# Kernel tuning notes

Hardware: AMD Instinct MI355X
Metric: run time of the kernel (lower is better)

Reference implementation:

```python
import jax, jax.numpy as jnp
import numpy as np

B, N, DIM, H, DH = 4, 2048, 1024, 16, 64

def setup_inputs() -> dict:
    key = jax.random.key(0)
    k1, k2, k3 = jax.random.split(key, 3)
    x = jax.random.normal(k1, (B, N, DIM), dtype=jnp.float32)
    mask = jnp.ones((B, N), dtype=bool)
    w_qkv = jax.random.normal(k2, (DIM, 3 * H * DH), dtype=jnp.float32) * (DIM ** -0.5)
    w_out = jax.random.normal(k3, (H * DH, DIM), dtype=jnp.float32) * ((H * DH) ** -0.5)
    b_out = jnp.zeros((DIM,), dtype=jnp.float32)
    return {"x": x, "mask": mask, "w_qkv": w_qkv, "w_out": w_out, "b_out": b_out}

def reference(x, mask, w_qkv, w_out, b_out):
    b, n, _ = x.shape
    h, dh = H, DH
    scale = dh ** -0.5
    qkv = x @ w_qkv  # [b, n, 3*h*dh]
    q, k, v = jnp.split(qkv, 3, axis=-1)
    # [b, n, h*dh] -> [b, h, n, dh]
    reshape = lambda t: t.reshape(b, n, h, dh).transpose(0, 2, 1, 3)
    q, k, v = reshape(q) * scale, reshape(k), reshape(v)
    dots = jnp.einsum('bhid,bhjd->bhij', q, k)  # materialized N x N scores
    neg = -jnp.finfo(dots.dtype).max
    # key padding mask: [b, j] -> [b, 1, 1, j]
    dots = jnp.where(mask[:, None, None, :], dots, neg)
    # causal mask: mask out j > i
    causal = jnp.triu(jnp.ones((n, n), dtype=bool), k=1)
    dots = jnp.where(causal[None, None, :, :], neg, dots)
    attn = jax.nn.softmax(dots, axis=-1)
    out = jnp.einsum('bhij,bhjd->bhid', attn, v)
    out = out.transpose(0, 2, 1, 3).reshape(b, n, h * dh)
    return out @ w_out + b_out
```

## Files before the change

kernel.cpp:

```cpp
#include <hip/hip_runtime.h>

#define B_   4
#define N_   2048
#define DIM_ 1024
#define H_   16
#define DH_  64
#define NT   (B_ * N_)
#define PS   ((size_t)B_ * H_ * N_ * DH_)

typedef __bf16 bf16x8 __attribute__((ext_vector_type(8)));
typedef short  s16x4  __attribute__((ext_vector_type(4)));
typedef float  f32x4  __attribute__((ext_vector_type(4)));
typedef unsigned int   u32;
typedef unsigned int   u32x2 __attribute__((ext_vector_type(2)));
typedef unsigned short u16;

#define LOG2E 1.44269504088896f
#define QSCALE (0.125f * LOG2E)

__device__ __forceinline__ u16 f2bf(float f) {
  u32 u = __float_as_uint(f);
  u += 0x7FFFu + ((u >> 16) & 1u);
  return (u16)(u >> 16);
}

__device__ __forceinline__ u32 bfpack(float f0, float f1) {
  u32 a = __float_as_uint(f0) + 0x8000u;
  u32 b = __float_as_uint(f1) + 0x8000u;
  return __builtin_amdgcn_perm(b, a, 0x07060302);
}

__device__ __forceinline__ float fexp2(float x) {
  return __builtin_amdgcn_exp2f(x);
}

__device__ __forceinline__ f32x4 mfma32(bf16x8 a, bf16x8 b, f32x4 c) {
  return __builtin_amdgcn_mfma_f32_16x16x32_bf16(a, b, c, 0, 0, 0);
}
__device__ __forceinline__ f32x4 mfma16k(s16x4 a, s16x4 b, f32x4 c) {
  return __builtin_amdgcn_mfma_f32_16x16x16bf16_1k(a, b, c, 0, 0, 0);
}

__device__ __forceinline__ void gld16(const void* g, void* l) {
  __builtin_amdgcn_global_load_lds(
      (const __attribute__((address_space(1))) u32*)g,
      (__attribute__((address_space(3))) u32*)l, 16, 0, 0);
}

__device__ __forceinline__ void transpose_body(
    const float* __restrict__ w, u16* __restrict__ wt,
    int K, int Ncols, int bx, int by, int tid, u16* T ) {
  const int n0 = bx * 64, k0 = by * 64;
  const int r = tid >> 4, c4 = (tid & 15) * 4;
#pragma unroll
  for (int i = 0; i < 4; ++i) {
    int row = r + i * 16;
    float4 f = *(const float4*)(w + (size_t)(k0 + row) * Ncols + n0 + c4);
    u16* p = &T[row * 66 + c4];
    p[0] = f2bf(f.x); p[1] = f2bf(f.y); p[2] = f2bf(f.z); p[3] = f2bf(f.w);
  }
  __syncthreads();
  const int nr = tid >> 2, kc = (tid & 3) * 16;
  u32 p[8];
#pragma unroll
  for (int j = 0; j < 8; ++j)
    p[j] = (u32)T[(kc + 2 * j) * 66 + nr] | ((u32)T[(kc + 2 * j + 1) * 66 + nr] << 16);
  size_t dst = (size_t)(n0 + nr) * K + k0 + kc;
  *(uint4*)(wt + dst)     = make_uint4(p[0], p[1], p[2], p[3]);
  *(uint4*)(wt + dst + 8) = make_uint4(p[4], p[5], p[6], p[7]);
}

__global__ __launch_bounds__(256) void prologue_kernel(
    const float* __restrict__ x, u16* __restrict__ xb,
    const float* __restrict__ w_qkv, u16* __restrict__ wqkvT,
    const float* __restrict__ w_out, u16* __restrict__ woutT) {
  __shared__ u16 T[64 * 66];
  const int b = blockIdx.x, tid = threadIdx.x;
  if (b < 4096) {
    size_t i = ((size_t)b * 256 + tid) * 8;
    float4 f0 = *(const float4*)(x + i);
    float4 f1 = *(const float4*)(x + i + 4);
    uint4 o;
    o.x = (u32)f2bf(f0.x) | ((u32)f2bf(f0.y) << 16);
    o.y = (u32)f2bf(f0.z) | ((u32)f2bf(f0.w) << 16);
    o.z = (u32)f2bf(f1.x) | ((u32)f2bf(f1.y) << 16);
    o.w = (u32)f2bf(f1.z) | ((u32)f2bf(f1.w) << 16);
    *(uint4*)(xb + i) = o;
  } else if (b < 4864) {
    int idx = b - 4096;
    transpose_body(w_qkv, wqkvT, 1024, 3072, idx % 48, idx / 48, tid, T);
  } else {
    int idx = b - 4864;
    transpose_body(w_out, woutT, 1024, 1024, idx % 16, idx / 16, tid, T);
  }
}

__global__ __launch_bounds__(256) void qkv_gemm_kernel(
    const u16* __restrict__ xb, const u16* __restrict__ wt,
    u16* __restrict__ q, u16* __restrict__ k, u16* __restrict__ vt) {
  __shared__ alignas(16) u16 As[2 * 128 * 64];
  __shared__ alignas(16) u16 Bs[2 * 128 * 64];
  const int tid = threadIdx.x, wave = tid >> 6, lane = tid & 63;
  const int quad = lane >> 4, l15 = lane & 15;
  const int wm = (wave >> 1) * 64, wn = (wave & 1) * 64;
  const int m0 = blockIdx.y * 128, n0 = blockIdx.x * 128;
  const int srow = lane >> 3;
  const int schunk = (lane & 7) ^ srow;

  const u16* asrc = xb + (size_t)(m0 + srow) * DIM_ + schunk * 8;
  const u16* bsrc = wt + (size_t)(n0 + srow) * DIM_ + schunk * 8;

  f32x4 acc[4][4] = {};

#pragma unroll
  for (int i = 0; i < 4; ++i) {
    int c = wave * 4 + i;
    gld16(asrc + (size_t)(c * 8) * DIM_, As + c * 512);
    gld16(bsrc + (size_t)(c * 8) * DIM_, Bs + c * 512);
  }

  for (int t = 0; t < 16; ++t) {
    if (t < 15) {
      int pn = (t + 1) & 1;
#pragma unroll
      for (int i = 0; i < 4; ++i) {
        int c = wave * 4 + i;
        gld16(asrc + (size_t)(c * 8) * DIM_ + (t + 1) * 64, As + pn * 8192 + c * 512);
        gld16(bsrc + (size_t)(c * 8) * DIM_ + (t + 1) * 64, Bs + pn * 8192 + c * 512);
      }
      asm volatile("s_waitcnt vmcnt(8)" ::: "memory");
    } else {
      asm volatile("s_waitcnt vmcnt(0)" ::: "memory");
    }
    __builtin_amdgcn_s_barrier();
    __builtin_amdgcn_sched_barrier(0);

    const u16* Ab = As + (t & 1) * 8192;
    const u16* Bb = Bs + (t & 1) * 8192;
#pragma unroll
    for (int h = 0; h < 2; ++h) {
      bf16x8 af[4], bfr[4];
#pragma unroll
      for (int mi = 0; mi < 4; ++mi) {
        int row = wm + mi * 16 + l15;
        af[mi] = *(const bf16x8*)(Ab + row * 64 + (((quad + 4 * h) ^ (row & 7)) * 8));
      }
#pragma unroll
      for (int ni = 0; ni < 4; ++ni) {
        int row = wn + ni * 16 + l15;
        bfr[ni] = *(const bf16x8*)(Bb + row * 64 + (((quad + 4 * h) ^ (row & 7)) * 8));
      }
#pragma unroll
      for (int ni = 0; ni < 4; ++ni)
#pragma unroll
        for (int mi = 0; mi < 4; ++mi)
          acc[mi][ni] = mfma32(af[mi], bfr[ni], acc[mi][ni]);
    }
    __builtin_amdgcn_sched_barrier(0);
    __builtin_amdgcn_s_barrier();
  }

#pragma unroll
  for (int ni = 0; ni < 4; ++ni) {
    int colg = n0 + wn + ni * 16 + l15;
    int part = colg >> 10, rem = colg & 1023;
    int hh = rem >> 6, d = rem & 63;
#pragma unroll
    for (int mi = 0; mi < 4; ++mi) {
      int row0 = m0 + wm + mi * 16 + quad * 4;
      int bb = row0 >> 11, nn0 = row0 & 2047;
      size_t bh = (size_t)(bb * H_ + hh);
      if (part == 0) {
#pragma unroll
        for (int r = 0; r < 4; ++r)
          q[(bh * N_ + nn0 + r) * DH_ + d] = f2bf(acc[mi][ni][r] * QSCALE);
      } else if (part == 1) {
#pragma unroll
        for (int r = 0; r < 4; ++r)
          k[(bh * N_ + nn0 + r) * DH_ + d] = f2bf(acc[mi][ni][r]);
      } else {
        u32 lo = bfpack(acc[mi][ni][0], acc[mi][ni][1]);
        u32 hi = bfpack(acc[mi][ni][2], acc[mi][ni][3]);
        *(uint2*)(vt + (bh * DH_ + d) * N_ + nn0) = make_uint2(lo, hi);
      }
    }
  }
}

__global__ __launch_bounds__(512, 8) void attn_kernel(
    const u16* __restrict__ q, const u16* __restrict__ k,
    const u16* __restrict__ vt, u16* __restrict__ ctx) {
  __shared__ alignas(16) u16 Ks[2 * 64 * 64];
  __shared__ alignas(16) u16 Vs[2 * 64 * 64];
  const int tid = threadIdx.x, wave = tid >> 6, lane = tid & 63;
  const int quad = lane >> 4, l15 = lane & 15;
  const int head = blockIdx.x;
  const int p = blockIdx.y;
  const int hh = head & 15, bb = head >> 4;
  const int wgrp = wave >> 2, wsub = wave & 3;
  const int qt = wgrp ? (31 - p) : p;

  const size_t bhofs = (size_t)(bb * H_ + hh) << 17;
  const u16* qp = q + bhofs;
  const u16* kp = k + bhofs;
  const u16* vp = vt + bhofs;

  const int row = qt * 64 + wsub * 16 + l15;
  const bf16x8 qf0 = *(const bf16x8*)(qp + (size_t)row * 64 + quad * 8);
  const bf16x8 qf1 = *(const bf16x8*)(qp + (size_t)row * 64 + 32 + quad * 8);

  float l_s = 0.f;
  f32x4 o[4] = {};

  const int srow8 = lane >> 3;
  const int sslot = (lane & 7) ^ srow8;
  const u16* kstage = kp + (size_t)(wave * 8 + srow8) * 64 + sslot * 8;
  const u16* vstage = vp + (size_t)(wave * 8 + srow8) * N_ + sslot * 8;

  const int smax = 31 - p;

  gld16(kstage, Ks + wave * 512);
  gld16(vstage, Vs + wave * 512);

  for (int s = 0; s <= smax; ++s) {
    if (s < smax) {
      int pn = (s + 1) & 1;
      gld16(kstage + (size_t)(s + 1) * 4096, Ks + pn * 4096 + wave * 512);
      gld16(vstage + (size_t)(s + 1) * 64,   Vs + pn * 4096 + wave * 512);
      asm volatile("s_waitcnt vmcnt(2)" ::: "memory");
    } else {
      asm volatile("s_waitcnt vmcnt(0)" ::: "memory");
    }
    __builtin_amdgcn_s_barrier();
    __builtin_amdgcn_sched_barrier(0);

    if (s <= qt) {
      const int h = s & 1;
      const int kbm = (s == qt) ? wsub : 3;
      const bool needmask = (s == qt);
      const int rowrel = row - s * 64;
      const u16* Kh = Ks + h * 4096;
      const u16* Vh = Vs + h * 4096;
#pragma unroll
      for (int kb = 0; kb < 4; ++kb) {
        if (kb <= kbm) {
          int rk = kb * 16 + l15;
          bf16x8 k0 = *(const bf16x8*)(Kh + rk * 64 + ((quad ^ (rk & 7)) * 8));
          bf16x8 k1 = *(const bf16x8*)(Kh + rk * 64 + (((quad + 4) ^ (rk & 7)) * 8));
          f32x4 z = {};
          z = mfma32(k0, qf0, z);
          z = mfma32(k1, qf1, z);
          if (needmask) {
#pragma unroll
            for (int r = 0; r < 4; ++r)
              if (kb * 16 + quad * 4 + r > rowrel) z[r] = -INFINITY;
          }
          float p0 = fexp2(z[0]), p1 = fexp2(z[1]);
          float p2 = fexp2(z[2]), p3 = fexp2(z[3]);
          l_s += (p0 + p1) + (p2 + p3);
          u32x2 pp = {bfpack(p0, p1), bfpack(p2, p3)};
          s16x4 pbv = __builtin_bit_cast(s16x4, pp);
          int f = 2 * kb + (quad >> 1);
#pragma unroll
          for (int db = 0; db < 4; ++db) {
            int rv = db * 16 + l15;
            int ch = f ^ (rv & 7);
            s16x4 vf = *(const s16x4*)(Vh + rv * 64 + ch * 8 + (quad & 1) * 4);
            o[db] = mfma16k(vf, pbv, o[db]);
          }
        }
      }
    }
    __builtin_amdgcn_sched_barrier(0);
    __builtin_amdgcn_s_barrier();
  }

  l_s += __shfl_xor(l_s, 16);
  l_s += __shfl_xor(l_s, 32);

  {
    float inv = 1.0f / l_s;
    int token = bb * N_ + row;
#pragma unroll
    for (int db = 0; db < 4; ++db) {
      u32 lo = bfpack(o[db][0] * inv, o[db][1] * inv);
      u32 hi = bfpack(o[db][2] * inv, o[db][3] * inv);
      *(uint2*)(ctx + (size_t)token * DIM_ + hh * DH_ + db * 16 + quad * 4) =
          make_uint2(lo, hi);
    }
  }
}

__global__ __launch_bounds__(256) void out_gemm_kernel(
    const u16* __restrict__ cb, const u16* __restrict__ wt,
    const float* __restrict__ bias, float* __restrict__ out) {
  __shared__ alignas(16) u16 As[2 * 128 * 64];
  __shared__ alignas(16) u16 Bs[2 * 128 * 64];
  const int tid = threadIdx.x, wave = tid >> 6, lane = tid & 63;
  const int quad = lane >> 4, l15 = lane & 15;
  const int wm = (wave >> 1) * 64, wn = (wave & 1) * 64;
  const int m0 = blockIdx.y * 128, n0 = blockIdx.x * 128;
  const int srow = lane >> 3;
  const int schunk = (lane & 7) ^ srow;

  const u16* asrc = cb + (size_t)(m0 + srow) * DIM_ + schunk * 8;
  const u16* bsrc = wt + (size_t)(n0 + srow) * DIM_ + schunk * 8;

  f32x4 acc[4][4] = {};

#pragma unroll
  for (int i = 0; i < 4; ++i) {
    int c = wave * 4 + i;
    gld16(asrc + (size_t)(c * 8) * DIM_, As + c * 512);
    gld16(bsrc + (size_t)(c * 8) * DIM_, Bs + c * 512);
  }

  for (int t = 0; t < 16; ++t) {
    if (t < 15) {
      int pn = (t + 1) & 1;
#pragma unroll
      for (int i = 0; i < 4; ++i) {
        int c = wave * 4 + i;
        gld16(asrc + (size_t)(c * 8) * DIM_ + (t + 1) * 64, As + pn * 8192 + c * 512);
        gld16(bsrc + (size_t)(c * 8) * DIM_ + (t + 1) * 64, Bs + pn * 8192 + c * 512);
      }
      asm volatile("s_waitcnt vmcnt(8)" ::: "memory");
    } else {
      asm volatile("s_waitcnt vmcnt(0)" ::: "memory");
    }
    __builtin_amdgcn_s_barrier();
    __builtin_amdgcn_sched_barrier(0);

    const u16* Ab = As + (t & 1) * 8192;
    const u16* Bb = Bs + (t & 1) * 8192;
#pragma unroll
    for (int h = 0; h < 2; ++h) {
      bf16x8 af[4], bfr[4];
#pragma unroll
      for (int mi = 0; mi < 4; ++mi) {
        int row = wm + mi * 16 + l15;
        af[mi] = *(const bf16x8*)(Ab + row * 64 + (((quad + 4 * h) ^ (row & 7)) * 8));
      }
#pragma unroll
      for (int ni = 0; ni < 4; ++ni) {
        int row = wn + ni * 16 + l15;
        bfr[ni] = *(const bf16x8*)(Bb + row * 64 + (((quad + 4 * h) ^ (row & 7)) * 8));
      }
#pragma unroll
      for (int ni = 0; ni < 4; ++ni)
#pragma unroll
        for (int mi = 0; mi < 4; ++mi)
          acc[mi][ni] = mfma32(af[mi], bfr[ni], acc[mi][ni]);
    }
    __builtin_amdgcn_sched_barrier(0);
    __builtin_amdgcn_s_barrier();
  }

#pragma unroll
  for (int ni = 0; ni < 4; ++ni) {
    int col = n0 + wn + ni * 16 + l15;
    float bv = bias[col];
#pragma unroll
    for (int mi = 0; mi < 4; ++mi) {
      int row0 = m0 + wm + mi * 16 + quad * 4;
#pragma unroll
      for (int r = 0; r < 4; ++r)
        out[(size_t)(row0 + r) * DIM_ + col] = acc[mi][ni][r] + bv;
    }
  }
}

extern "C" void kernel_launch(void* const* d_in, const int* in_sizes, int n_in,
                              void* d_out, int out_size, void* d_ws, size_t ws_size,
                              hipStream_t stream) {
  (void)in_sizes; (void)n_in; (void)out_size; (void)ws_size;
  const float* x     = (const float*)d_in[0];
  const float* w_qkv = (const float*)d_in[2];
  const float* w_out = (const float*)d_in[3];
  const float* b_out = (const float*)d_in[4];
  float* out = (float*)d_out;

  u16* xb_ctx = (u16*)d_ws;
  u16* qw     = xb_ctx + (size_t)NT * DIM_;
  u16* kw     = qw + PS;
  u16* vw     = kw + PS;
  u16* wqkvT  = vw + PS;
  u16* woutT  = wqkvT + (size_t)3072 * 1024;

  prologue_kernel<<<5120, 256, 0, stream>>>(x, xb_ctx, w_qkv, wqkvT, w_out, woutT);
  qkv_gemm_kernel<<<dim3(24, 64), 256, 0, stream>>>(xb_ctx, wqkvT, qw, kw, vw);
  attn_kernel<<<dim3(64, 16), 512, 0, stream>>>(qw, kw, vw, xb_ctx);
  out_gemm_kernel<<<dim3(8, 64), 256, 0, stream>>>(xb_ctx, woutT, b_out, out);
}
```

Before: 244.5 us.

## Enlarge QKV GEMM tile to 256x256 with 8 waves and interleaved prefetch

The QKV projection GEMM moves from 128x128 tiles with 4 waves to 256x256 tiles with 8 waves, doubling reuse of each LDS tile and halving global traffic per output. The K-loop is split into four sub-phases: each issues one slice of the next tile's global-to-LDS loads between fragment reads and an MFMA burst, and the MFMA bursts run at raised wave priority (setprio). The grid drops to 384 blocks, which risks under-filling the GPU's compute units. The extra barriers per iteration and the larger accumulator array also add sync and register pressure.

```diff
diff --git a/kernel.cpp b/kernel.cpp
--- a/kernel.cpp
+++ b/kernel.cpp
@@ -95,92 +95,100 @@
   }
 }
 
-__global__ __launch_bounds__(256) void qkv_gemm_kernel(
+__global__ __launch_bounds__(512, 2) void qkv_gemm_kernel(
     const u16* __restrict__ xb, const u16* __restrict__ wt,
     u16* __restrict__ q, u16* __restrict__ k, u16* __restrict__ vt) {
-  __shared__ alignas(16) u16 As[2 * 128 * 64];
-  __shared__ alignas(16) u16 Bs[2 * 128 * 64];
+  __shared__ alignas(16) u16 As[2 * 256 * 64];
+  __shared__ alignas(16) u16 Bs[2 * 256 * 64];
   const int tid = threadIdx.x, wave = tid >> 6, lane = tid & 63;
   const int quad = lane >> 4, l15 = lane & 15;
-  const int wm = (wave >> 1) * 64, wn = (wave & 1) * 64;
-  const int m0 = blockIdx.y * 128, n0 = blockIdx.x * 128;
+  const int wr = wave >> 2, wc = wave & 3;
+  const int m0 = blockIdx.y * 256, n0 = blockIdx.x * 256;
   const int srow = lane >> 3;
   const int schunk = (lane & 7) ^ srow;
 
   const u16* asrc = xb + (size_t)(m0 + srow) * DIM_ + schunk * 8;
   const u16* bsrc = wt + (size_t)(n0 + srow) * DIM_ + schunk * 8;
 
-  f32x4 acc[4][4] = {};
-
-#pragma unroll
-  for (int i = 0; i < 4; ++i) {
-    int c = wave * 4 + i;
+  f32x4 acc[8][4] = {};
+
+#pragma unroll
+  for (int j = 0; j < 4; ++j) {
+    int c = wave * 4 + j;
     gld16(asrc + (size_t)(c * 8) * DIM_, As + c * 512);
     gld16(bsrc + (size_t)(c * 8) * DIM_, Bs + c * 512);
   }
 
   for (int t = 0; t < 16; ++t) {
-    if (t < 15) {
-      int pn = (t + 1) & 1;
-#pragma unroll
-      for (int i = 0; i < 4; ++i) {
-        int c = wave * 4 + i;
-        gld16(asrc + (size_t)(c * 8) * DIM_ + (t + 1) * 64, As + pn * 8192 + c * 512);
-        gld16(bsrc + (size_t)(c * 8) * DIM_ + (t + 1) * 64, Bs + pn * 8192 + c * 512);
-      }
-      asm volatile("s_waitcnt vmcnt(8)" ::: "memory");
-    } else {
-      asm volatile("s_waitcnt vmcnt(0)" ::: "memory");
-    }
+    asm volatile("s_waitcnt vmcnt(0)" ::: "memory");
     __builtin_amdgcn_s_barrier();
     __builtin_amdgcn_sched_barrier(0);
 
-    const u16* Ab = As + (t & 1) * 8192;
-    const u16* Bb = Bs + (t & 1) * 8192;
-#pragma unroll
-    for (int h = 0; h < 2; ++h) {
-      bf16x8 af[4], bfr[4];
-#pragma unroll
-      for (int mi = 0; mi < 4; ++mi) {
-        int row = wm + mi * 16 + l15;
-        af[mi] = *(const bf16x8*)(Ab + row * 64 + (((quad + 4 * h) ^ (row & 7)) * 8));
-      }
-#pragma unroll
-      for (int ni = 0; ni < 4; ++ni) {
-        int row = wn + ni * 16 + l15;
-        bfr[ni] = *(const bf16x8*)(Bb + row * 64 + (((quad + 4 * h) ^ (row & 7)) * 8));
-      }
-#pragma unroll
-      for (int ni = 0; ni < 4; ++ni)
-#pragma unroll
-        for (int mi = 0; mi < 4; ++mi)
-          acc[mi][ni] = mfma32(af[mi], bfr[ni], acc[mi][ni]);
-    }
-    __builtin_amdgcn_sched_barrier(0);
-    __builtin_amdgcn_s_barrier();
+    const u16* Ab = As + (t & 1) * 16384;
+    const u16* Bb = Bs + (t & 1) * 16384;
+    const int pn = (t + 1) & 1;
+    bf16x8 bfr[4][2];
+#pragma unroll
+    for (int p = 0; p < 4; ++p) {
+      if (p == 0) {
+#pragma unroll
+        for (int ni = 0; ni < 4; ++ni) {
+          int rowb = wc * 64 + ni * 16 + l15;
+#pragma unroll
+          for (int h = 0; h < 2; ++h)
+            bfr[ni][h] = *(const bf16x8*)(Bb + rowb * 64 + (((quad + 4 * h) ^ (rowb & 7)) * 8));
+        }
+      }
+      bf16x8 af[2][2];
+#pragma unroll
+      for (int mi = 0; mi < 2; ++mi) {
+        int rowa = wr * 128 + p * 32 + mi * 16 + l15;
+#pragma unroll
+        for (int h = 0; h < 2; ++h)
+          af[mi][h] = *(const bf16x8*)(Ab + rowa * 64 + (((quad + 4 * h) ^ (rowa & 7)) * 8));
+      }
+      if (t < 15) {
+        int c = wave * 4 + p;
+        gld16(asrc + (size_t)(c * 8) * DIM_ + (t + 1) * 64, As + pn * 16384 + c * 512);
+        gld16(bsrc + (size_t)(c * 8) * DIM_ + (t + 1) * 64, Bs + pn * 16384 + c * 512);
+      }
+      __builtin_amdgcn_s_barrier();
+      __builtin_amdgcn_s_setprio(1);
+      __builtin_amdgcn_sched_barrier(0);
+#pragma unroll
+      for (int h = 0; h < 2; ++h)
+#pragma unroll
+        for (int ni = 0; ni < 4; ++ni)
+#pragma unroll
+          for (int mi = 0; mi < 2; ++mi)
+            acc[p * 2 + mi][ni] = mfma32(af[mi][h], bfr[ni][h], acc[p * 2 + mi][ni]);
+      __builtin_amdgcn_sched_barrier(0);
+      __builtin_amdgcn_s_setprio(0);
+      __builtin_amdgcn_s_barrier();
+    }
   }
 
 #pragma unroll
   for (int ni = 0; ni < 4; ++ni) {
-    int colg = n0 + wn + ni * 16 + l15;
+    int colg = n0 + wc * 64 + ni * 16 + l15;
     int part = colg >> 10, rem = colg & 1023;
     int hh = rem >> 6, d = rem & 63;
 #pragma unroll
-    for (int mi = 0; mi < 4; ++mi) {
-      int row0 = m0 + wm + mi * 16 + quad * 4;
+    for (int mg = 0; mg < 8; ++mg) {
+      int row0 = m0 + wr * 128 + mg * 16 + quad * 4;
       int bb = row0 >> 11, nn0 = row0 & 2047;
       size_t bh = (size_t)(bb * H_ + hh);
       if (part == 0) {
 #pragma unroll
         for (int r = 0; r < 4; ++r)
-          q[(bh * N_ + nn0 + r) * DH_ + d] = f2bf(acc[mi][ni][r] * QSCALE);
+          q[(bh * N_ + nn0 + r) * DH_ + d] = f2bf(acc[mg][ni][r] * QSCALE);
       } else if (part == 1) {
 #pragma unroll
         for (int r = 0; r < 4; ++r)
-          k[(bh * N_ + nn0 + r) * DH_ + d] = f2bf(acc[mi][ni][r]);
+          k[(bh * N_ + nn0 + r) * DH_ + d] = f2bf(acc[mg][ni][r]);
       } else {
-        u32 lo = bfpack(acc[mi][ni][0], acc[mi][ni][1]);
-        u32 hi = bfpack(acc[mi][ni][2], acc[mi][ni][3]);
+        u32 lo = bfpack(acc[mg][ni][0], acc[mg][ni][1]);
+        u32 hi = bfpack(acc[mg][ni][2], acc[mg][ni][3]);
         *(uint2*)(vt + (bh * DH_ + d) * N_ + nn0) = make_uint2(lo, hi);
       }
     }
@@ -388,7 +396,7 @@
   u16* woutT  = wqkvT + (size_t)3072 * 1024;
 
   prologue_kernel<<<5120, 256, 0, stream>>>(x, xb_ctx, w_qkv, wqkvT, w_out, woutT);
-  qkv_gemm_kernel<<<dim3(24, 64), 256, 0, stream>>>(xb_ctx, wqkvT, qw, kw, vw);
+  qkv_gemm_kernel<<<dim3(12, 32), 512, 0, stream>>>(xb_ctx, wqkvT, qw, kw, vw);
   attn_kernel<<<dim3(64, 16), 512, 0, stream>>>(qw, kw, vw, xb_ctx);
   out_gemm_kernel<<<dim3(8, 64), 256, 0, stream>>>(xb_ctx, woutT, b_out, out);
 }
```

New measurement: 257.4 us. 1.05x slower.
